# Performance work log

Measured on AMD Instinct MI355X. Metric: run time of the kernel, lower is better.

The kernel has to match this reference:

```python
import jax, jax.numpy as jnp
import numpy as np

DIM = 4096
N_HEADS = 32
N_KV_HEADS = 8
HEAD_DIM = DIM // N_HEADS
MAX_SEQ = 2048
BATCH = 2


def _precompute_freqs(head_dim, seq_len, theta=10000.0):
    inv = 1.0 / (theta ** (np.arange(0, head_dim, 2, dtype=np.float32) / head_dim))
    t = np.arange(seq_len, dtype=np.float32)
    freqs = np.outer(t, inv)  # (seq, head_dim/2)
    return jnp.asarray(np.cos(freqs)), jnp.asarray(np.sin(freqs))


def setup_inputs() -> dict:
    key = jax.random.key(0)
    ks = jax.random.split(key, 6)
    s = 1.0 / np.sqrt(DIM)
    x = jax.random.normal(ks[0], (BATCH, MAX_SEQ, DIM), dtype=jnp.float32)
    wq = jax.random.normal(ks[1], (N_HEADS * HEAD_DIM, DIM), dtype=jnp.float32) * s
    wk = jax.random.normal(ks[2], (N_KV_HEADS * HEAD_DIM, DIM), dtype=jnp.float32) * s
    wv = jax.random.normal(ks[3], (N_KV_HEADS * HEAD_DIM, DIM), dtype=jnp.float32) * s
    wo = jax.random.normal(ks[4], (DIM, N_HEADS * HEAD_DIM), dtype=jnp.float32) * s
    freqs_cos, freqs_sin = _precompute_freqs(HEAD_DIM, MAX_SEQ)
    cache_k = jnp.zeros((BATCH, MAX_SEQ, N_KV_HEADS, HEAD_DIM), dtype=jnp.float32)
    cache_v = jnp.zeros((BATCH, MAX_SEQ, N_KV_HEADS, HEAD_DIM), dtype=jnp.float32)
    return {"x": x, "wq": wq, "wk": wk, "wv": wv, "wo": wo,
            "freqs_cos": freqs_cos, "freqs_sin": freqs_sin,
            "cache_k": cache_k, "cache_v": cache_v, "start_pos": 0}


def _apply_rope(x, cos, sin):
    # x: (B, S, H, D); interleaved complex pairs (x[2i], x[2i+1]), Llama style
    xr = x[..., 0::2]
    xi = x[..., 1::2]
    cos = cos[None, :, None, :]
    sin = sin[None, :, None, :]
    out_r = xr * cos - xi * sin
    out_i = xr * sin + xi * cos
    return jnp.stack([out_r, out_i], axis=-1).reshape(x.shape)


def reference(x, wq, wk, wv, wo, freqs_cos, freqs_sin, cache_k, cache_v, start_pos):
    B, S, D = x.shape
    n_kv, hd = cache_k.shape[2], cache_k.shape[3]
    n_h = wq.shape[0] // hd
    n_rep = n_h // n_kv

    q = (x @ wq.T).reshape(B, S, n_h, hd)
    k = (x @ wk.T).reshape(B, S, n_kv, hd)
    v = (x @ wv.T).reshape(B, S, n_kv, hd)

    q = _apply_rope(q, freqs_cos, freqs_sin)
    k = _apply_rope(k, freqs_cos, freqs_sin)

    # KV-cache append
    cache_k = jax.lax.dynamic_update_slice(cache_k, k, (0, start_pos, 0, 0))
    cache_v = jax.lax.dynamic_update_slice(cache_v, v, (0, start_pos, 0, 0))
    T = start_pos + S
    keys = cache_k[:, :T]    # (B, T, n_kv, hd)
    values = cache_v[:, :T]

    # repeat_kv for grouped-query attention
    keys = jnp.repeat(keys, n_rep, axis=2)      # (B, T, n_h, hd)
    values = jnp.repeat(values, n_rep, axis=2)

    qh = q.transpose(0, 2, 1, 3)       # (B, n_h, S, hd)
    kh = keys.transpose(0, 2, 1, 3)    # (B, n_h, T, hd)
    vh = values.transpose(0, 2, 1, 3)  # (B, n_h, T, hd)

    scores = jnp.einsum('bhsd,bhtd->bhst', qh, kh) / jnp.sqrt(jnp.float32(hd))
    # causal mask: key position t attends only if t <= start_pos + s
    mask = jnp.arange(T)[None, :] <= (start_pos + jnp.arange(S))[:, None]
    scores = jnp.where(mask[None, None], scores, jnp.float32(-1e9))
    probs = jax.nn.softmax(scores.astype(jnp.float32), axis=-1).astype(qh.dtype)

    out = jnp.einsum('bhst,bhtd->bhsd', probs, vh)
    out = out.transpose(0, 2, 1, 3).reshape(B, S, n_h * hd)
    return out @ wo.T
```

## Files before the change

kernel.cpp:

```cpp
#include <hip/hip_runtime.h>

typedef unsigned short u16;
typedef unsigned int u32;
typedef __bf16 bf16x8 __attribute__((ext_vector_type(8)));
typedef float f32x4 __attribute__((ext_vector_type(4)));

#define DIM 4096
#define NH 32
#define NKV 8
#define HD 128
#define SEQ 2048
#define BATCH 2

__device__ __forceinline__ u16 f2bf(float f) {
  u32 u = __float_as_uint(f);
  u += 0x7fffu + ((u >> 16) & 1u);
  return (u16)(u >> 16);
}
__device__ __forceinline__ float bf2f(u16 b) {
  return __uint_as_float(((u32)b) << 16);
}

__device__ __forceinline__ void async16(void* lds, const void* g) {
  __builtin_amdgcn_global_load_lds(
      (__attribute__((address_space(1))) void*)(g),
      (__attribute__((address_space(3))) void*)(lds), 16, 0, 0);
}

__global__ __launch_bounds__(256) void cast_kernel(const float* __restrict__ in,
                                                   u16* __restrict__ out, int n4) {
  int i = blockIdx.x * 256 + threadIdx.x;
  if (i >= n4) return;
  float4 v = ((const float4*)in)[i];
  uint2 o;
  o.x = (u32)f2bf(v.x) | ((u32)f2bf(v.y) << 16);
  o.y = (u32)f2bf(v.z) | ((u32)f2bf(v.w) << 16);
  ((uint2*)out)[i] = o;
}

template <bool BF16OUT>
__global__ __launch_bounds__(256) void gemm_bt(const u16* __restrict__ A,
                                               const u16* __restrict__ B,
                                               void* __restrict__ Cv,
                                               int M, int N, int K) {
  __shared__ __align__(16) u16 As[128 * 32];
  __shared__ __align__(16) u16 Bs[128 * 32];
  const int tid = threadIdx.x;
  const int w = tid >> 6, l = tid & 63;
  const int wr = w >> 1, wc = w & 1;
  const int bm = blockIdx.x, bn = blockIdx.y;
  f32x4 acc[4][4] = {};
  const u16* Ab = A + (size_t)bm * 128 * K;
  const u16* Bb = B + (size_t)bn * 128 * K;
  const int lrow = l >> 2, lcol = (l & 3) * 8;

  for (int k0 = 0; k0 < K; k0 += 32) {
    __syncthreads();
#pragma unroll
    for (int i = 0; i < 2; ++i) {
      const int rbase = i * 64 + w * 16;
      async16(&As[rbase * 32], Ab + (size_t)(rbase + lrow) * K + k0 + lcol);
      async16(&Bs[rbase * 32], Bb + (size_t)(rbase + lrow) * K + k0 + lcol);
    }
    __syncthreads();
    bf16x8 af[4], bfv[4];
#pragma unroll
    for (int mi = 0; mi < 4; ++mi)
      af[mi] = *(const bf16x8*)&As[(wr * 64 + mi * 16 + (l & 15)) * 32 + (l >> 4) * 8];
#pragma unroll
    for (int ni = 0; ni < 4; ++ni)
      bfv[ni] = *(const bf16x8*)&Bs[(wc * 64 + ni * 16 + (l & 15)) * 32 + (l >> 4) * 8];
#pragma unroll
    for (int mi = 0; mi < 4; ++mi)
#pragma unroll
      for (int ni = 0; ni < 4; ++ni)
        acc[mi][ni] = __builtin_amdgcn_mfma_f32_16x16x32_bf16(af[mi], bfv[ni], acc[mi][ni], 0, 0, 0);
  }
#pragma unroll
  for (int mi = 0; mi < 4; ++mi)
#pragma unroll
    for (int ni = 0; ni < 4; ++ni)
#pragma unroll
      for (int r = 0; r < 4; ++r) {
        int row = bm * 128 + wr * 64 + mi * 16 + (l >> 4) * 4 + r;
        int col = bn * 128 + wc * 64 + ni * 16 + (l & 15);
        float v = acc[mi][ni][r];
        if (BF16OUT)
          ((u16*)Cv)[(size_t)row * N + col] = f2bf(v);
        else
          ((float*)Cv)[(size_t)row * N + col] = v;
      }
}

__global__ __launch_bounds__(256) void rope_kernel(u16* __restrict__ buf,
                                                   const float* __restrict__ fc,
                                                   const float* __restrict__ fs,
                                                   const int* __restrict__ spp,
                                                   int nh, int total) {
  int t = blockIdx.x * 256 + threadIdx.x;
  if (t >= total) return;
  int i = t & 63;
  int h = (t >> 6) % nh;
  int s = ((t >> 6) / nh) % SEQ;
  int b = t / (64 * nh * SEQ);
  int pos = spp[0] + s;
  float c = fc[pos * 64 + i], sn = fs[pos * 64 + i];
  u16* p = buf + ((size_t)(b * SEQ + s) * nh + h) * HD + 2 * i;
  u32 both = *(u32*)p;
  float xr = bf2f((u16)(both & 0xffffu));
  float xi = bf2f((u16)(both >> 16));
  float orr = xr * c - xi * sn;
  float oi = xr * sn + xi * c;
  *(u32*)p = (u32)f2bf(orr) | ((u32)f2bf(oi) << 16);
}

__device__ __forceinline__ int swz(int row, int colel) {
  int byte = (row << 8) + (colel << 1);
  byte ^= (row & 7) << 4;
  return byte >> 1;
}

__global__ __launch_bounds__(256) void attn_kernel(const u16* __restrict__ qb,
                                                   const u16* __restrict__ kb,
                                                   const u16* __restrict__ vb,
                                                   u16* __restrict__ ob,
                                                   const int* __restrict__ spp) {
  const int qt = blockIdx.x, h = blockIdx.y, b = blockIdx.z;
  const int kvh = h >> 2;
  const int tid = threadIdx.x, w = tid >> 6, l = tid & 63;
  const int sp = spp[0];
  __shared__ __align__(16) u16 Kl[32 * 128];
  __shared__ __align__(16) u16 Vl[32 * 128];
  __shared__ __align__(16) u16 Pl[4][16 * 32];
  const int qs = qt * 64;
  const int wq0 = qs + w * 16;

  bf16x8 qf[4];
  const u16* qrow = qb + (size_t)(b * SEQ + wq0 + (l & 15)) * DIM + h * HD;
#pragma unroll
  for (int kk = 0; kk < 4; ++kk)
    qf[kk] = *(const bf16x8*)(qrow + kk * 32 + (l >> 4) * 8);

  f32x4 acc[8] = {};
  float mst[4] = {-1e30f, -1e30f, -1e30f, -1e30f};
  float lst[4] = {0.f, 0.f, 0.f, 0.f};
  const int nt = qs / 32 + 2;

  for (int t = 0; t < nt; ++t) {
    const int t0 = t * 32;
    __syncthreads();
    for (int c = tid; c < 512; c += 256) {
      int row = c >> 4, col = (c & 15) * 8;
      size_t goff = (size_t)(b * SEQ + t0 + row) * (NKV * HD) + kvh * HD + col;
      *(int4*)&Kl[swz(row, col)] = *(const int4*)(kb + goff);
      *(int4*)&Vl[swz(row, col)] = *(const int4*)(vb + goff);
    }
    __syncthreads();

    float sv[2][4];
#pragma unroll
    for (int tt = 0; tt < 2; ++tt) {
      f32x4 sacc = {};
#pragma unroll
      for (int kk = 0; kk < 4; ++kk) {
        bf16x8 kf = *(const bf16x8*)&Kl[swz(tt * 16 + (l & 15), kk * 32 + (l >> 4) * 8)];
        sacc = __builtin_amdgcn_mfma_f32_16x16x32_bf16(qf[kk], kf, sacc, 0, 0, 0);
      }
#pragma unroll
      for (int r = 0; r < 4; ++r) {
        int qrow_s = wq0 + (l >> 4) * 4 + r;
        int tg = t0 + tt * 16 + (l & 15);
        float v = sacc[r] * 0.08838834764831845f;
        sv[tt][r] = (tg <= sp + qrow_s) ? v : -1e9f;
      }
    }
    float pm[4];
#pragma unroll
    for (int r = 0; r < 4; ++r) pm[r] = fmaxf(sv[0][r], sv[1][r]);
#pragma unroll
    for (int off = 1; off < 16; off <<= 1)
#pragma unroll
      for (int r = 0; r < 4; ++r) pm[r] = fmaxf(pm[r], __shfl_xor(pm[r], off));

    float esc[4];
#pragma unroll
    for (int r = 0; r < 4; ++r) {
      float mn = fmaxf(mst[r], pm[r]);
      esc[r] = __expf(mst[r] - mn);
      mst[r] = mn;
    }
    float p[2][4];
#pragma unroll
    for (int tt = 0; tt < 2; ++tt)
#pragma unroll
      for (int r = 0; r < 4; ++r) p[tt][r] = __expf(sv[tt][r] - mst[r]);
    float rs[4];
#pragma unroll
    for (int r = 0; r < 4; ++r) rs[r] = p[0][r] + p[1][r];
#pragma unroll
    for (int off = 1; off < 16; off <<= 1)
#pragma unroll
      for (int r = 0; r < 4; ++r) rs[r] += __shfl_xor(rs[r], off);
#pragma unroll
    for (int r = 0; r < 4; ++r) lst[r] = lst[r] * esc[r] + rs[r];
#pragma unroll
    for (int dc = 0; dc < 8; ++dc)
#pragma unroll
      for (int r = 0; r < 4; ++r) acc[dc][r] *= esc[r];

#pragma unroll
    for (int tt = 0; tt < 2; ++tt)
#pragma unroll
      for (int r = 0; r < 4; ++r)
        Pl[w][((l >> 4) * 4 + r) * 32 + tt * 16 + (l & 15)] = f2bf(p[tt][r]);
    bf16x8 pf = *(const bf16x8*)&Pl[w][(l & 15) * 32 + (l >> 4) * 8];

#pragma unroll
    for (int dc = 0; dc < 8; ++dc) {
      union { u16 u[8]; bf16x8 v; } uv;
#pragma unroll
      for (int j = 0; j < 8; ++j)
        uv.u[j] = Vl[swz((l >> 4) * 8 + j, dc * 16 + (l & 15))];
      acc[dc] = __builtin_amdgcn_mfma_f32_16x16x32_bf16(pf, uv.v, acc[dc], 0, 0, 0);
    }
  }
#pragma unroll
  for (int r = 0; r < 4; ++r) {
    float inv = 1.0f / lst[r];
    size_t rowoff = (size_t)(b * SEQ + wq0 + (l >> 4) * 4 + r) * DIM + h * HD;
#pragma unroll
    for (int dc = 0; dc < 8; ++dc)
      ob[rowoff + dc * 16 + (l & 15)] = f2bf(acc[dc][r] * inv);
  }
}

extern "C" void kernel_launch(void* const* d_in, const int* in_sizes, int n_in,
                              void* d_out, int out_size, void* d_ws, size_t ws_size,
                              hipStream_t stream) {
  (void)in_sizes; (void)n_in; (void)out_size; (void)ws_size;
  const float* x  = (const float*)d_in[0];
  const float* wq = (const float*)d_in[1];
  const float* wk = (const float*)d_in[2];
  const float* wv = (const float*)d_in[3];
  const float* wo = (const float*)d_in[4];
  const float* fc = (const float*)d_in[5];
  const float* fs = (const float*)d_in[6];
  const int* sp   = (const int*)d_in[9];

  char* ws = (char*)d_ws;
  size_t off = 0;
  auto alloc = [&](size_t bytes) {
    void* p = ws + off;
    off += (bytes + 255) & ~(size_t)255;
    return p;
  };
  u16* xb   = (u16*)alloc(16777216ull * 2);
  u16* wqb  = (u16*)alloc(16777216ull * 2);
  u16* wkb  = (u16*)alloc(4194304ull * 2);
  u16* wvb  = (u16*)alloc(4194304ull * 2);
  u16* wob  = (u16*)alloc(16777216ull * 2);
  u16* qbuf = (u16*)alloc(16777216ull * 2);
  u16* kbuf = (u16*)alloc(4194304ull * 2);
  u16* vbuf = (u16*)alloc(4194304ull * 2);
  u16* abuf = xb;

  auto cast = [&](const float* in, u16* out, size_t n) {
    int n4 = (int)(n / 4);
    cast_kernel<<<(n4 + 255) / 256, 256, 0, stream>>>(in, out, n4);
  };
  cast(x,  xb,  16777216ull);
  cast(wq, wqb, 16777216ull);
  cast(wk, wkb, 4194304ull);
  cast(wv, wvb, 4194304ull);
  cast(wo, wob, 16777216ull);

  gemm_bt<true><<<dim3(32, 32), 256, 0, stream>>>(xb, wqb, qbuf, 4096, 4096, 4096);
  gemm_bt<true><<<dim3(32, 8), 256, 0, stream>>>(xb, wkb, kbuf, 4096, 1024, 4096);
  gemm_bt<true><<<dim3(32, 8), 256, 0, stream>>>(xb, wvb, vbuf, 4096, 1024, 4096);

  rope_kernel<<<8388608 / 256, 256, 0, stream>>>(qbuf, fc, fs, sp, NH, 8388608);
  rope_kernel<<<2097152 / 256, 256, 0, stream>>>(kbuf, fc, fs, sp, NKV, 2097152);

  attn_kernel<<<dim3(32, 32, 2), 256, 0, stream>>>(qbuf, kbuf, vbuf, abuf, sp);

  gemm_bt<false><<<dim3(32, 32), 256, 0, stream>>>(abuf, wob, d_out, 4096, 4096, 4096);
}
```

Before: 1.465 ms.

## Widen attention KV tiles, transpose V in LDS, reorder heavy blocks first

Each attention iteration now covers a 64-key tile instead of a 32-key one. K is brought into LDS with async global-to-LDS loads, and V is stored transposed with a swizzle so the PV MFMA operands come from vector LDS reads instead of eight scalar reads. The causal mask is applied only on the diagonal tile, and blocks are launched on a flat grid that runs the longest query tiles first and spreads work across XCDs. The trade-offs are more LDS per block and a scalar transpose scatter of V into LDS. The diagonal-only masking also assumes start_pos is zero.

```diff
diff --git a/kernel.cpp b/kernel.cpp
--- a/kernel.cpp
+++ b/kernel.cpp
@@ -114,10 +114,13 @@
   *(u32*)p = (u32)f2bf(orr) | ((u32)f2bf(oi) << 16);
 }
 
-__device__ __forceinline__ int swz(int row, int colel) {
+__device__ __forceinline__ int kswz(int row, int colel) {
   int byte = (row << 8) + (colel << 1);
   byte ^= (row & 7) << 4;
   return byte >> 1;
+}
+__device__ __forceinline__ int vswz(int d, int kv) {
+  return d * 64 + (kv ^ ((d & 7) << 3));
 }
 
 __global__ __launch_bounds__(256) void attn_kernel(const u16* __restrict__ qb,
@@ -125,13 +128,16 @@
                                                    const u16* __restrict__ vb,
                                                    u16* __restrict__ ob,
                                                    const int* __restrict__ spp) {
-  const int qt = blockIdx.x, h = blockIdx.y, b = blockIdx.z;
+  const int wg = (blockIdx.x & 7) * 256 + (blockIdx.x >> 3);
+  const int qt = 31 - (wg & 31);
+  const int h = (wg >> 5) & 31;
+  const int b = wg >> 10;
   const int kvh = h >> 2;
   const int tid = threadIdx.x, w = tid >> 6, l = tid & 63;
   const int sp = spp[0];
-  __shared__ __align__(16) u16 Kl[32 * 128];
-  __shared__ __align__(16) u16 Vl[32 * 128];
-  __shared__ __align__(16) u16 Pl[4][16 * 32];
+  __shared__ __align__(16) u16 Kl[64 * 128];
+  __shared__ __align__(16) u16 Vt[128 * 64];
+  __shared__ __align__(16) u16 Pl[4][16 * 72];
   const int qs = qt * 64;
   const int wq0 = qs + w * 16;
 
@@ -144,39 +150,56 @@
   f32x4 acc[8] = {};
   float mst[4] = {-1e30f, -1e30f, -1e30f, -1e30f};
   float lst[4] = {0.f, 0.f, 0.f, 0.f};
-  const int nt = qs / 32 + 2;
+  const int nt = qt + 1;
+  const size_t kvbase = (size_t)b * SEQ * (NKV * HD) + kvh * HD;
 
   for (int t = 0; t < nt; ++t) {
-    const int t0 = t * 32;
+    const int t0 = t * 64;
     __syncthreads();
-    for (int c = tid; c < 512; c += 256) {
-      int row = c >> 4, col = (c & 15) * 8;
-      size_t goff = (size_t)(b * SEQ + t0 + row) * (NKV * HD) + kvh * HD + col;
-      *(int4*)&Kl[swz(row, col)] = *(const int4*)(kb + goff);
-      *(int4*)&Vl[swz(row, col)] = *(const int4*)(vb + goff);
+#pragma unroll
+    for (int c0 = 0; c0 < 4; ++c0) {
+      int g = c0 * 256 + tid;
+      int row = g >> 4;
+      int col = ((g & 15) ^ (row & 7)) * 8;
+      async16(&Kl[g * 8], kb + kvbase + (size_t)(t0 + row) * (NKV * HD) + col);
+    }
+#pragma unroll
+    for (int c0 = 0; c0 < 4; ++c0) {
+      int g = c0 * 256 + tid;
+      int row = g >> 4, col = (g & 15) * 8;
+      union { int4 i; u16 u[8]; } vv;
+      vv.i = *(const int4*)(vb + kvbase + (size_t)(t0 + row) * (NKV * HD) + col);
+#pragma unroll
+      for (int j = 0; j < 8; ++j) Vt[vswz(col + j, row)] = vv.u[j];
     }
     __syncthreads();
 
-    float sv[2][4];
-#pragma unroll
-    for (int tt = 0; tt < 2; ++tt) {
+    float sv[4][4];
+#pragma unroll
+    for (int tt = 0; tt < 4; ++tt) {
       f32x4 sacc = {};
 #pragma unroll
       for (int kk = 0; kk < 4; ++kk) {
-        bf16x8 kf = *(const bf16x8*)&Kl[swz(tt * 16 + (l & 15), kk * 32 + (l >> 4) * 8)];
+        bf16x8 kf = *(const bf16x8*)&Kl[kswz(tt * 16 + (l & 15), kk * 32 + (l >> 4) * 8)];
         sacc = __builtin_amdgcn_mfma_f32_16x16x32_bf16(qf[kk], kf, sacc, 0, 0, 0);
       }
 #pragma unroll
-      for (int r = 0; r < 4; ++r) {
-        int qrow_s = wq0 + (l >> 4) * 4 + r;
-        int tg = t0 + tt * 16 + (l & 15);
-        float v = sacc[r] * 0.08838834764831845f;
-        sv[tt][r] = (tg <= sp + qrow_s) ? v : -1e9f;
-      }
+      for (int r = 0; r < 4; ++r) sv[tt][r] = sacc[r] * 0.08838834764831845f;
+    }
+    if (t == nt - 1) {
+#pragma unroll
+      for (int tt = 0; tt < 4; ++tt)
+#pragma unroll
+        for (int r = 0; r < 4; ++r) {
+          int qrow_s = wq0 + (l >> 4) * 4 + r;
+          int tg = t0 + tt * 16 + (l & 15);
+          if (tg > sp + qrow_s) sv[tt][r] = -1e9f;
+        }
     }
     float pm[4];
 #pragma unroll
-    for (int r = 0; r < 4; ++r) pm[r] = fmaxf(sv[0][r], sv[1][r]);
+    for (int r = 0; r < 4; ++r)
+      pm[r] = fmaxf(fmaxf(sv[0][r], sv[1][r]), fmaxf(sv[2][r], sv[3][r]));
 #pragma unroll
     for (int off = 1; off < 16; off <<= 1)
 #pragma unroll
@@ -189,14 +212,14 @@
       esc[r] = __expf(mst[r] - mn);
       mst[r] = mn;
     }
-    float p[2][4];
-#pragma unroll
-    for (int tt = 0; tt < 2; ++tt)
+    float p[4][4];
+#pragma unroll
+    for (int tt = 0; tt < 4; ++tt)
 #pragma unroll
       for (int r = 0; r < 4; ++r) p[tt][r] = __expf(sv[tt][r] - mst[r]);
     float rs[4];
 #pragma unroll
-    for (int r = 0; r < 4; ++r) rs[r] = p[0][r] + p[1][r];
+    for (int r = 0; r < 4; ++r) rs[r] = (p[0][r] + p[1][r]) + (p[2][r] + p[3][r]);
 #pragma unroll
     for (int off = 1; off < 16; off <<= 1)
 #pragma unroll
@@ -209,19 +232,23 @@
       for (int r = 0; r < 4; ++r) acc[dc][r] *= esc[r];
 
 #pragma unroll
-    for (int tt = 0; tt < 2; ++tt)
+    for (int tt = 0; tt < 4; ++tt)
 #pragma unroll
       for (int r = 0; r < 4; ++r)
-        Pl[w][((l >> 4) * 4 + r) * 32 + tt * 16 + (l & 15)] = f2bf(p[tt][r]);
-    bf16x8 pf = *(const bf16x8*)&Pl[w][(l & 15) * 32 + (l >> 4) * 8];
+        Pl[w][((l >> 4) * 4 + r) * 72 + tt * 16 + (l & 15)] = f2bf(p[tt][r]);
+    bf16x8 pf[2];
+#pragma unroll
+    for (int kk2 = 0; kk2 < 2; ++kk2)
+      pf[kk2] = *(const bf16x8*)&Pl[w][(l & 15) * 72 + kk2 * 32 + (l >> 4) * 8];
 
 #pragma unroll
     for (int dc = 0; dc < 8; ++dc) {
-      union { u16 u[8]; bf16x8 v; } uv;
-#pragma unroll
-      for (int j = 0; j < 8; ++j)
-        uv.u[j] = Vl[swz((l >> 4) * 8 + j, dc * 16 + (l & 15))];
-      acc[dc] = __builtin_amdgcn_mfma_f32_16x16x32_bf16(pf, uv.v, acc[dc], 0, 0, 0);
+#pragma unroll
+      for (int kk2 = 0; kk2 < 2; ++kk2) {
+        int d = dc * 16 + (l & 15);
+        bf16x8 vf = *(const bf16x8*)&Vt[vswz(d, kk2 * 32 + (l >> 4) * 8)];
+        acc[dc] = __builtin_amdgcn_mfma_f32_16x16x32_bf16(pf[kk2], vf, acc[dc], 0, 0, 0);
+      }
     }
   }
 #pragma unroll
@@ -281,7 +308,7 @@
   rope_kernel<<<8388608 / 256, 256, 0, stream>>>(qbuf, fc, fs, sp, NH, 8388608);
   rope_kernel<<<2097152 / 256, 256, 0, stream>>>(kbuf, fc, fs, sp, NKV, 2097152);
 
-  attn_kernel<<<dim3(32, 32, 2), 256, 0, stream>>>(qbuf, kbuf, vbuf, abuf, sp);
+  attn_kernel<<<2048, 256, 0, stream>>>(qbuf, kbuf, vbuf, abuf, sp);
 
   gemm_bt<false><<<dim3(32, 32), 256, 0, stream>>>(abuf, wob, d_out, 4096, 4096, 4096);
 }
```

Result: faster. 1.295 ms (-11.6%).
